# Kernel tuning notes

Hardware: AMD Instinct MI355X
Metric: run time of the kernel (lower is better)

The kernel has to match this reference:

```python
import math
import jax, jax.numpy as jnp
import numpy as np

C = 32        # per-head dim
N_HEAD = 8
C_IN = 128

def setup_inputs() -> dict:
    key = jax.random.key(0)
    ks = jax.random.split(key, 10)
    B, S = 1, 256
    sc = 0.05  # keep logits in a sane range
    x    = jax.random.normal(ks[0], (B, S, S, C_IN), dtype=jnp.float32)
    bias = jax.random.normal(ks[1], (B, N_HEAD, S, S), dtype=jnp.float32)
    attention_mask = jax.random.randint(ks[2], (B, S, S), 0, 2).astype(bool)
    Wq = jax.random.normal(ks[3], (C_IN, C * N_HEAD), dtype=jnp.float32) * sc
    Wk = jax.random.normal(ks[4], (C_IN, C * N_HEAD), dtype=jnp.float32) * sc
    Wv = jax.random.normal(ks[5], (C_IN, C * N_HEAD), dtype=jnp.float32) * sc
    Wo = jax.random.normal(ks[6], (C * N_HEAD, C_IN), dtype=jnp.float32) * sc
    bo = jnp.zeros((C_IN,), dtype=jnp.float32)
    Wg = jax.random.normal(ks[7], (C_IN, C * N_HEAD), dtype=jnp.float32) * sc
    bg = jnp.zeros((C * N_HEAD,), dtype=jnp.float32)
    return {"x": x, "bias": bias, "attention_mask": attention_mask,
            "Wq": Wq, "Wk": Wk, "Wv": Wv, "Wo": Wo, "bo": bo, "Wg": Wg, "bg": bg}

def reference(x, bias, attention_mask, Wq, Wk, Wv, Wo, bo, Wg, bg):
    # x: [B, S, L, c_in]; attn_dim=2 is already the second-to-last dim,
    # so the torch movedim(attn_dim, -2) is the identity here.
    B, S, L, _ = x.shape
    q = x @ Wq  # [B, S, L, H*c]
    k = x @ Wk
    v = x @ Wv
    # split heads: [B, S, L, H, c] -> [B, S, H, L, c]
    def split_heads(t):
        return t.reshape(B, S, L, N_HEAD, C).transpose(0, 1, 3, 2, 4)
    q, k, v = split_heads(q), split_heads(k), split_heads(v)
    q = q / math.sqrt(C)
    # attention logits: [B, S, H, q, k]
    a = jnp.einsum('bshqc,bshkc->bshqk', q, k)
    # bias [B, H, q, k] -> broadcast over the axial batch dim S
    a = a + bias[:, None, :, :, :]
    # mask [B, S, k] -> [B, S, 1, 1, k]; masked positions get -inf
    m = attention_mask[:, :, None, None, :]
    a = jnp.where(m, a, -jnp.inf)
    a = jax.nn.softmax(a, axis=-1)
    o = jnp.einsum('bshqk,bshkc->bshqc', a, v)
    # merge heads: [B, S, H, L, c] -> [B, S, L, H*c]
    o = o.transpose(0, 1, 3, 2, 4).reshape(B, S, L, N_HEAD * C)
    # sigmoid gate
    g = jax.nn.sigmoid(x @ Wg + bg)
    o = g * o
    return o @ Wo + bo
```

## Files before the change

kernel.cpp:

```cpp
#include <hip/hip_runtime.h>
#include <hip/hip_bf16.h>
#include <cstdint>

#define CIN 128
#define NH 8
#define CH 32

typedef short bf16x8 __attribute__((ext_vector_type(8)));
typedef short bf16x4 __attribute__((ext_vector_type(4)));
typedef float f32x4 __attribute__((ext_vector_type(4)));

__device__ __forceinline__ short f2bf(float f) {
  union { float f; unsigned u; } v; v.f = f;
  unsigned r = (v.u + 0x7FFFu + ((v.u >> 16) & 1u)) >> 16;
  return (short)r;
}
__device__ __forceinline__ float bf2f(short s) {
  union { unsigned u; float f; } v; v.u = ((unsigned)(unsigned short)s) << 16;
  return v.f;
}
__device__ __forceinline__ unsigned pk2bf(float a, float b) {
  union { __hip_bfloat162 h; unsigned u; } cv;
  cv.h = __float22bfloat162_rn(make_float2(a, b));
  return cv.u;
}

__global__ __launch_bounds__(256) void prep(
    const float* __restrict__ Wq, const float* __restrict__ Wk,
    const float* __restrict__ Wv, const float* __restrict__ Wg,
    const float* __restrict__ Wo,
    const uint4* __restrict__ mask,
    short* __restrict__ WT, short* __restrict__ WoT,
    unsigned int* __restrict__ flag)
{
  const int b = blockIdx.x;
  const int tid = threadIdx.x;
  if (b < 40) {
    __shared__ short tile[64 * 68];
    const int rr = tid >> 4;
    const int cc = tid & 15;
    if (b < 32) {
      const int seg = b >> 3, sub = b & 7, kt = sub >> 2, nt = sub & 3;
      const int k0 = kt * 64, n0 = nt * 64;
      const float* W = (seg == 0) ? Wq : (seg == 1) ? Wk : (seg == 2) ? Wv : Wg;
      const float qs = (seg == 0) ? 0.17677669529663689f : 1.0f;
#pragma unroll
      for (int p = 0; p < 4; ++p) {
        int r = p * 16 + rr;
        float4 a = *(const float4*)(W + (size_t)(k0 + r) * 256 + n0 + cc * 4);
        tile[r * 68 + cc * 4 + 0] = f2bf(a.x * qs);
        tile[r * 68 + cc * 4 + 1] = f2bf(a.y * qs);
        tile[r * 68 + cc * 4 + 2] = f2bf(a.z * qs);
        tile[r * 68 + cc * 4 + 3] = f2bf(a.w * qs);
      }
      __syncthreads();
#pragma unroll
      for (int p = 0; p < 4; ++p) {
        int rn = p * 16 + rr;
        bf16x4 v;
        v[0] = tile[(cc * 4 + 0) * 68 + rn];
        v[1] = tile[(cc * 4 + 1) * 68 + rn];
        v[2] = tile[(cc * 4 + 2) * 68 + rn];
        v[3] = tile[(cc * 4 + 3) * 68 + rn];
        *(bf16x4*)(WT + (size_t)(seg * 256 + n0 + rn) * 128 + k0 + cc * 4) = v;
      }
    } else {
      const int sub = b - 32, kt = sub >> 1, nt = sub & 1;
      const int k0 = kt * 64, n0 = nt * 64;
#pragma unroll
      for (int p = 0; p < 4; ++p) {
        int r = p * 16 + rr;
        float4 a = *(const float4*)(Wo + (size_t)(k0 + r) * 128 + n0 + cc * 4);
        tile[r * 68 + cc * 4 + 0] = f2bf(a.x);
        tile[r * 68 + cc * 4 + 1] = f2bf(a.y);
        tile[r * 68 + cc * 4 + 2] = f2bf(a.z);
        tile[r * 68 + cc * 4 + 3] = f2bf(a.w);
      }
      __syncthreads();
#pragma unroll
      for (int p = 0; p < 4; ++p) {
        int rn = p * 16 + rr;
        bf16x4 v;
        v[0] = tile[(cc * 4 + 0) * 68 + rn];
        v[1] = tile[(cc * 4 + 1) * 68 + rn];
        v[2] = tile[(cc * 4 + 2) * 68 + rn];
        v[3] = tile[(cc * 4 + 3) * 68 + rn];
        *(bf16x4*)(WoT + (size_t)(n0 + rn) * 256 + k0 + cc * 4) = v;
      }
    }
  } else {
    __shared__ int viol;
    if (tid == 0) viol = 0;
    __syncthreads();
    int v = 0;
#pragma unroll
    for (int j = 0; j < 16; ++j) {
      uint4 w = mask[j * 256 + tid];
      v |= (w.x > 1u) | (w.y > 1u) | (w.z > 1u) | (w.w > 1u);
    }
    if (v) atomicOr(&viol, 1);
    __syncthreads();
    if (tid == 0) *flag = viol ? 0u : 1u;
  }
}

__global__ __launch_bounds__(512) void fused_attn(
    const float* __restrict__ x, const short* __restrict__ WT,
    const short* __restrict__ WoT,
    const float* __restrict__ bias, const float* __restrict__ bg,
    const float* __restrict__ bo,
    const void* __restrict__ maskraw, const unsigned int* __restrict__ flagp,
    float* __restrict__ out)
{
  __shared__ __align__(16) short xl[256 * 136];
  __shared__ __align__(16) short kL[256 * 40];
  __shared__ __align__(16) short vL[32 * 264];
  __shared__ __align__(16) short qL[256 * 40];
  __shared__ float lL[256];
  __shared__ unsigned int scratch[8];

  const int tid = threadIdx.x;
  const int srow = blockIdx.x;
  const int lane = tid & 63, w = tid >> 6;
  const int g = lane >> 4, c16 = lane & 15;
  const int myrow = w * 32;

  const unsigned int fl = *flagp;
  if (tid < 256) {
    int mv = fl ? ((const int*)maskraw)[srow * 256 + tid]
                : (int)((const unsigned char*)maskraw)[srow * 256 + tid];
    unsigned long long bb = __ballot(mv != 0);
    if (lane == 0) {
      scratch[w * 2 + 0] = (unsigned int)bb;
      scratch[w * 2 + 1] = (unsigned int)(bb >> 32);
    }
  }

  {
    const float* xs = x + (size_t)srow * 256 * 128;
#pragma unroll
    for (int it = 0; it < 16; ++it) {
      int idx = it * 512 + tid;
      int row = idx >> 5, c4 = idx & 31;
      float4 a = *(const float4*)(xs + (size_t)idx * 4);
      union { unsigned u[2]; bf16x4 v; } pu;
      pu.u[0] = pk2bf(a.x, a.y);
      pu.u[1] = pk2bf(a.z, a.w);
      *(bf16x4*)&xl[row * 136 + c4 * 4] = pu.v;
    }
  }
  __syncthreads();

  unsigned int mb[8];
#pragma unroll
  for (int j = 0; j < 8; ++j) mb[j] = scratch[j];

  const f32x4 zero4 = {0.f, 0.f, 0.f, 0.f};
  f32x4 acc_out[2][8];
#pragma unroll
  for (int qt = 0; qt < 2; ++qt)
#pragma unroll
    for (int ct = 0; ct < 8; ++ct) acc_out[qt][ct] = zero4;

#pragma unroll 1
  for (int h = 0; h < 8; ++h) {
    f32x4 ga[2][2];
    {
      f32x4 acc[2][2];
#pragma unroll
      for (int ct = 0; ct < 2; ++ct)
#pragma unroll
        for (int rt = 0; rt < 2; ++rt) acc[ct][rt] = zero4;
#pragma unroll
      for (int kk = 0; kk < 4; ++kk) {
        bf16x8 wf[2], xf[2];
#pragma unroll
        for (int ct = 0; ct < 2; ++ct)
          wf[ct] = *(const bf16x8*)(WT + (size_t)(256 + h * CH + ct * 16 + c16) * 128 + kk * 32 + g * 8);
#pragma unroll
        for (int rt = 0; rt < 2; ++rt)
          xf[rt] = *(const bf16x8*)&xl[(myrow + rt * 16 + c16) * 136 + kk * 32 + g * 8];
#pragma unroll
        for (int ct = 0; ct < 2; ++ct)
#pragma unroll
          for (int rt = 0; rt < 2; ++rt)
            acc[ct][rt] = __builtin_amdgcn_mfma_f32_16x16x32_bf16(wf[ct], xf[rt], acc[ct][rt], 0, 0, 0);
      }
#pragma unroll
      for (int ct = 0; ct < 2; ++ct)
#pragma unroll
        for (int rt = 0; rt < 2; ++rt) {
          union { unsigned u[2]; bf16x4 v; } pu;
          pu.u[0] = pk2bf(acc[ct][rt][0], acc[ct][rt][1]);
          pu.u[1] = pk2bf(acc[ct][rt][2], acc[ct][rt][3]);
          *(bf16x4*)&kL[(myrow + rt * 16 + c16) * 40 + ct * 16 + g * 4] = pu.v;
        }
    }
    {
      f32x4 acc[2][2];
#pragma unroll
      for (int rt = 0; rt < 2; ++rt)
#pragma unroll
        for (int ct = 0; ct < 2; ++ct) acc[rt][ct] = zero4;
#pragma unroll
      for (int kk = 0; kk < 4; ++kk) {
        bf16x8 wf[2], xf[2];
#pragma unroll
        for (int ct = 0; ct < 2; ++ct)
          wf[ct] = *(const bf16x8*)(WT + (size_t)(512 + h * CH + ct * 16 + c16) * 128 + kk * 32 + g * 8);
#pragma unroll
        for (int rt = 0; rt < 2; ++rt)
          xf[rt] = *(const bf16x8*)&xl[(myrow + rt * 16 + c16) * 136 + kk * 32 + g * 8];
#pragma unroll
        for (int rt = 0; rt < 2; ++rt)
#pragma unroll
          for (int ct = 0; ct < 2; ++ct)
            acc[rt][ct] = __builtin_amdgcn_mfma_f32_16x16x32_bf16(xf[rt], wf[ct], acc[rt][ct], 0, 0, 0);
      }
#pragma unroll
      for (int rt = 0; rt < 2; ++rt)
#pragma unroll
        for (int ct = 0; ct < 2; ++ct) {
          union { unsigned u[2]; bf16x4 v; } pu;
          pu.u[0] = pk2bf(acc[rt][ct][0], acc[rt][ct][1]);
          pu.u[1] = pk2bf(acc[rt][ct][2], acc[rt][ct][3]);
          *(bf16x4*)&vL[(size_t)(ct * 16 + c16) * 264 + myrow + rt * 16 + g * 4] = pu.v;
        }
    }
    {
      f32x4 acc[2][2];
#pragma unroll
      for (int ct = 0; ct < 2; ++ct)
#pragma unroll
        for (int rt = 0; rt < 2; ++rt) acc[ct][rt] = zero4;
#pragma unroll
      for (int kk = 0; kk < 4; ++kk) {
        bf16x8 wf[2], xf[2];
#pragma unroll
        for (int ct = 0; ct < 2; ++ct)
          wf[ct] = *(const bf16x8*)(WT + (size_t)(0 + h * CH + ct * 16 + c16) * 128 + kk * 32 + g * 8);
#pragma unroll
        for (int rt = 0; rt < 2; ++rt)
          xf[rt] = *(const bf16x8*)&xl[(myrow + rt * 16 + c16) * 136 + kk * 32 + g * 8];
#pragma unroll
        for (int ct = 0; ct < 2; ++ct)
#pragma unroll
          for (int rt = 0; rt < 2; ++rt)
            acc[ct][rt] = __builtin_amdgcn_mfma_f32_16x16x32_bf16(wf[ct], xf[rt], acc[ct][rt], 0, 0, 0);
      }
#pragma unroll
      for (int ct = 0; ct < 2; ++ct)
#pragma unroll
        for (int rt = 0; rt < 2; ++rt) {
          union { unsigned u[2]; bf16x4 v; } pu;
          pu.u[0] = pk2bf(acc[ct][rt][0], acc[ct][rt][1]);
          pu.u[1] = pk2bf(acc[ct][rt][2], acc[ct][rt][3]);
          *(bf16x4*)&qL[(myrow + rt * 16 + c16) * 40 + ct * 16 + g * 4] = pu.v;
        }
    }
    {
#pragma unroll
      for (int rt = 0; rt < 2; ++rt)
#pragma unroll
        for (int ct = 0; ct < 2; ++ct) ga[rt][ct] = zero4;
#pragma unroll
      for (int kk = 0; kk < 4; ++kk) {
        bf16x8 wf[2], xf[2];
#pragma unroll
        for (int ct = 0; ct < 2; ++ct)
          wf[ct] = *(const bf16x8*)(WT + (size_t)(768 + h * CH + ct * 16 + c16) * 128 + kk * 32 + g * 8);
#pragma unroll
        for (int rt = 0; rt < 2; ++rt)
          xf[rt] = *(const bf16x8*)&xl[(myrow + rt * 16 + c16) * 136 + kk * 32 + g * 8];
#pragma unroll
        for (int rt = 0; rt < 2; ++rt)
#pragma unroll
          for (int ct = 0; ct < 2; ++ct)
            ga[rt][ct] = __builtin_amdgcn_mfma_f32_16x16x32_bf16(xf[rt], wf[ct], ga[rt][ct], 0, 0, 0);
      }
    }
    __syncthreads();

    const int qb = myrow;
    bf16x8 qf[2];
#pragma unroll
    for (int qt = 0; qt < 2; ++qt)
      qf[qt] = *(const bf16x8*)&qL[(qb + qt * 16 + c16) * 40 + g * 8];

    float l_[2] = {0.f, 0.f};
    f32x4 O[2][2];
#pragma unroll
    for (int qt = 0; qt < 2; ++qt) { O[qt][0] = zero4; O[qt][1] = zero4; }

    const float* bh = bias + (size_t)h * 65536;

#pragma unroll 1
    for (int ch = 0; ch < 8; ++ch) {
      float4 bb4[2][2];
#pragma unroll
      for (int kt = 0; kt < 2; ++kt)
#pragma unroll
        for (int qt = 0; qt < 2; ++qt)
          bb4[kt][qt] = *(const float4*)(bh + (size_t)(qb + qt * 16 + c16) * 256 +
                                         ch * 32 + kt * 16 + g * 4);

#pragma unroll
      for (int kt = 0; kt < 2; ++kt) {
        bf16x8 kf = *(const bf16x8*)&kL[(ch * 32 + kt * 16 + c16) * 40 + g * 8];
        bf16x4 vlo = *(const bf16x4*)&vL[(size_t)c16 * 264 + ch * 32 + kt * 16 + g * 4];
        bf16x4 vhi = *(const bf16x4*)&vL[(size_t)(16 + c16) * 264 + ch * 32 + kt * 16 + g * 4];
        const unsigned nib = (mb[ch] >> (kt * 16 + g * 4)) & 0xFu;
        float em[4];
#pragma unroll
        for (int i = 0; i < 4; ++i) em[i] = ((nib >> i) & 1u) ? 1.f : 0.f;
#pragma unroll
        for (int qt = 0; qt < 2; ++qt) {
          f32x4 S = __builtin_amdgcn_mfma_f32_16x16x32_bf16(kf, qf[qt], zero4, 0, 0, 0);
          float p0 = em[0] * __expf(fminf(S[0] + bb4[kt][qt].x, 85.f));
          float p1 = em[1] * __expf(fminf(S[1] + bb4[kt][qt].y, 85.f));
          float p2 = em[2] * __expf(fminf(S[2] + bb4[kt][qt].z, 85.f));
          float p3 = em[3] * __expf(fminf(S[3] + bb4[kt][qt].w, 85.f));
          l_[qt] += (p0 + p1) + (p2 + p3);
          union { unsigned u[2]; bf16x4 v; } pu;
          pu.u[0] = pk2bf(p0, p1);
          pu.u[1] = pk2bf(p2, p3);
          O[qt][0] = __builtin_amdgcn_mfma_f32_16x16x16bf16_1k(pu.v, vlo, O[qt][0], 0, 0, 0);
          O[qt][1] = __builtin_amdgcn_mfma_f32_16x16x16bf16_1k(pu.v, vhi, O[qt][1], 0, 0, 0);
        }
      }
    }

#pragma unroll
    for (int qt = 0; qt < 2; ++qt) {
      float v = l_[qt];
      v += __shfl_xor(v, 16);
      v += __shfl_xor(v, 32);
      if (lane < 16) lL[myrow + qt * 16 + c16] = v;
    }

    {
      float bgl0 = bg[h * CH + c16];
      float bgl1 = bg[h * CH + 16 + c16];
#pragma unroll
      for (int qt = 0; qt < 2; ++qt)
#pragma unroll
        for (int i = 0; i < 4; ++i) {
          int row = qb + qt * 16 + g * 4 + i;
          float inv = 1.f / lL[myrow + qt * 16 + g * 4 + i];
          float g0 = 1.f / (1.f + __expf(-(ga[qt][0][i] + bgl0)));
          float g1 = 1.f / (1.f + __expf(-(ga[qt][1][i] + bgl1)));
          qL[row * 40 + c16]      = f2bf(O[qt][0][i] * inv * g0);
          qL[row * 40 + 16 + c16] = f2bf(O[qt][1][i] * inv * g1);
        }
    }

    {
      bf16x8 wo[8];
#pragma unroll
      for (int ct = 0; ct < 8; ++ct)
        wo[ct] = *(const bf16x8*)(WoT + (size_t)(ct * 16 + c16) * 256 + h * 32 + g * 8);
#pragma unroll
      for (int qt = 0; qt < 2; ++qt) {
        bf16x8 of = *(const bf16x8*)&qL[(qb + qt * 16 + c16) * 40 + g * 8];
#pragma unroll
        for (int ct = 0; ct < 8; ++ct)
          acc_out[qt][ct] = __builtin_amdgcn_mfma_f32_16x16x32_bf16(of, wo[ct], acc_out[qt][ct], 0, 0, 0);
      }
    }
    __syncthreads();
  }

#pragma unroll
  for (int ct = 0; ct < 8; ++ct) {
    float bv = bo[ct * 16 + c16];
#pragma unroll
    for (int qt = 0; qt < 2; ++qt)
#pragma unroll
      for (int i = 0; i < 4; ++i)
        out[((size_t)srow * 256 + myrow + qt * 16 + g * 4 + i) * 128 + ct * 16 + c16] =
            acc_out[qt][ct][i] + bv;
  }
}

extern "C" void kernel_launch(void* const* d_in, const int* in_sizes, int n_in,
                              void* d_out, int out_size, void* d_ws, size_t ws_size,
                              hipStream_t stream) {
  const float* x    = (const float*)d_in[0];
  const float* bias = (const float*)d_in[1];
  const void*  mask = d_in[2];
  const float* Wq   = (const float*)d_in[3];
  const float* Wk   = (const float*)d_in[4];
  const float* Wv   = (const float*)d_in[5];
  const float* Wo   = (const float*)d_in[6];
  const float* bo   = (const float*)d_in[7];
  const float* Wg   = (const float*)d_in[8];
  const float* bg   = (const float*)d_in[9];
  float* out = (float*)d_out;

  unsigned int* flag = (unsigned int*)d_ws;
  short* WT  = (short*)((char*)d_ws + 256);
  short* WoT = WT + 131072;

  prep<<<41, 256, 0, stream>>>(Wq, Wk, Wv, Wg, Wo, (const uint4*)mask,
                               WT, WoT, flag);
  fused_attn<<<256, 512, 0, stream>>>(x, WT, WoT, bias, bg, bo,
                                      mask, flag, out);
}
```

Baseline: 239.6 us.

## Fuse weight prep into attention kernel via cooperative launch and grid sync

Merges the separate weight-transpose/bf16-conversion and mask-format check kernel into the main attention kernel. The first 41 blocks do the prep work, then all blocks meet at a cooperative-groups grid barrier before the attention phase. The goal is to remove one kernel launch and the inter-kernel gap. The cost is a grid-wide sync, and the code falls back to the two-kernel path if the cooperative launch fails.

```diff
diff --git a/kernel.cpp b/kernel.cpp
--- a/kernel.cpp
+++ b/kernel.cpp
@@ -1,5 +1,6 @@
 #include <hip/hip_runtime.h>
 #include <hip/hip_bf16.h>
+#include <hip/hip_cooperative_groups.h>
 #include <cstdint>
 
 #define CIN 128
@@ -104,13 +105,14 @@
   }
 }
 
-__global__ __launch_bounds__(512) void fused_attn(
-    const float* __restrict__ x, const short* __restrict__ WT,
-    const short* __restrict__ WoT,
-    const float* __restrict__ bias, const float* __restrict__ bg,
-    const float* __restrict__ bo,
-    const void* __restrict__ maskraw, const unsigned int* __restrict__ flagp,
-    float* __restrict__ out)
+__global__ __launch_bounds__(512) void fused_all(
+    const float* __restrict__ x, short* __restrict__ WT,
+    short* __restrict__ WoT, const float* __restrict__ bias,
+    const float* __restrict__ bg, const float* __restrict__ bo,
+    const void* __restrict__ maskraw, unsigned int* __restrict__ flagp,
+    const float* __restrict__ Wq, const float* __restrict__ Wk,
+    const float* __restrict__ Wv, const float* __restrict__ Wg,
+    const float* __restrict__ Wo, float* __restrict__ out, int do_prep)
 {
   __shared__ __align__(16) short xl[256 * 136];
   __shared__ __align__(16) short kL[256 * 40];
@@ -118,6 +120,7 @@
   __shared__ __align__(16) short qL[256 * 40];
   __shared__ float lL[256];
   __shared__ unsigned int scratch[8];
+  __shared__ int viol;
 
   const int tid = threadIdx.x;
   const int srow = blockIdx.x;
@@ -125,7 +128,81 @@
   const int g = lane >> 4, c16 = lane & 15;
   const int myrow = w * 32;
 
-  const unsigned int fl = *flagp;
+  if (do_prep) {
+    const int b = blockIdx.x;
+    if (b < 40) {
+      short* tile = xl;
+      const int rr = tid >> 4;
+      const int cc = tid & 15;
+      if (b < 32) {
+        const int seg = b >> 3, sub = b & 7, kt = sub >> 2, nt = sub & 3;
+        const int k0 = kt * 64, n0 = nt * 64;
+        const float* W = (seg == 0) ? Wq : (seg == 1) ? Wk : (seg == 2) ? Wv : Wg;
+        const float qs = (seg == 0) ? 0.17677669529663689f : 1.0f;
+#pragma unroll
+        for (int p = 0; p < 2; ++p) {
+          int r = p * 32 + rr;
+          float4 a = *(const float4*)(W + (size_t)(k0 + r) * 256 + n0 + cc * 4);
+          tile[r * 68 + cc * 4 + 0] = f2bf(a.x * qs);
+          tile[r * 68 + cc * 4 + 1] = f2bf(a.y * qs);
+          tile[r * 68 + cc * 4 + 2] = f2bf(a.z * qs);
+          tile[r * 68 + cc * 4 + 3] = f2bf(a.w * qs);
+        }
+        __syncthreads();
+#pragma unroll
+        for (int p = 0; p < 2; ++p) {
+          int rn = p * 32 + rr;
+          bf16x4 v;
+          v[0] = tile[(cc * 4 + 0) * 68 + rn];
+          v[1] = tile[(cc * 4 + 1) * 68 + rn];
+          v[2] = tile[(cc * 4 + 2) * 68 + rn];
+          v[3] = tile[(cc * 4 + 3) * 68 + rn];
+          *(bf16x4*)(WT + (size_t)(seg * 256 + n0 + rn) * 128 + k0 + cc * 4) = v;
+        }
+      } else {
+        const int sub = b - 32, kt = sub >> 1, nt = sub & 1;
+        const int k0 = kt * 64, n0 = nt * 64;
+#pragma unroll
+        for (int p = 0; p < 2; ++p) {
+          int r = p * 32 + rr;
+          float4 a = *(const float4*)(Wo + (size_t)(k0 + r) * 128 + n0 + cc * 4);
+          tile[r * 68 + cc * 4 + 0] = f2bf(a.x);
+          tile[r * 68 + cc * 4 + 1] = f2bf(a.y);
+          tile[r * 68 + cc * 4 + 2] = f2bf(a.z);
+          tile[r * 68 + cc * 4 + 3] = f2bf(a.w);
+        }
+        __syncthreads();
+#pragma unroll
+        for (int p = 0; p < 2; ++p) {
+          int rn = p * 32 + rr;
+          bf16x4 v;
+          v[0] = tile[(cc * 4 + 0) * 68 + rn];
+          v[1] = tile[(cc * 4 + 1) * 68 + rn];
+          v[2] = tile[(cc * 4 + 2) * 68 + rn];
+          v[3] = tile[(cc * 4 + 3) * 68 + rn];
+          *(bf16x4*)(WoT + (size_t)(n0 + rn) * 256 + k0 + cc * 4) = v;
+        }
+      }
+    } else if (b == 40) {
+      if (tid == 0) viol = 0;
+      __syncthreads();
+      int v = 0;
+      const uint4* m4 = (const uint4*)maskraw;
+#pragma unroll
+      for (int j = 0; j < 8; ++j) {
+        uint4 wv = m4[j * 512 + tid];
+        v |= (wv.x > 1u) | (wv.y > 1u) | (wv.z > 1u) | (wv.w > 1u);
+      }
+      if (v) atomicOr(&viol, 1);
+      __syncthreads();
+      if (tid == 0) *flagp = viol ? 0u : 1u;
+    }
+    __threadfence();
+    cooperative_groups::this_grid().sync();
+    __threadfence();
+  }
+
+  const unsigned int fl = *(volatile const unsigned int*)flagp;
   if (tid < 256) {
     int mv = fl ? ((const int*)maskraw)[srow * 256 + tid]
                 : (int)((const unsigned char*)maskraw)[srow * 256 + tid];
@@ -401,8 +478,18 @@
   short* WT  = (short*)((char*)d_ws + 256);
   short* WoT = WT + 131072;
 
-  prep<<<41, 256, 0, stream>>>(Wq, Wk, Wv, Wg, Wo, (const uint4*)mask,
-                               WT, WoT, flag);
-  fused_attn<<<256, 512, 0, stream>>>(x, WT, WoT, bias, bg, bo,
-                                      mask, flag, out);
-}
+  int do_prep = 1;
+  void* kargs[] = {
+    (void*)&x, (void*)&WT, (void*)&WoT, (void*)&bias, (void*)&bg, (void*)&bo,
+    (void*)&mask, (void*)&flag, (void*)&Wq, (void*)&Wk, (void*)&Wv, (void*)&Wg,
+    (void*)&Wo, (void*)&out, (void*)&do_prep
+  };
+  hipError_t err = hipLaunchCooperativeKernel(
+      reinterpret_cast<void*>(fused_all), dim3(256), dim3(512), kargs, 0, stream);
+  if (err != hipSuccess) {
+    prep<<<41, 256, 0, stream>>>(Wq, Wk, Wv, Wg, Wo, (const uint4*)mask,
+                                 WT, WoT, flag);
+    fused_all<<<256, 512, 0, stream>>>(x, WT, WoT, bias, bg, bo,
+                                       mask, flag, Wq, Wk, Wv, Wg, Wo, out, 0);
+  }
+}
```

After: 360.5 us. 1.5x slower.
